# Kernel tuning notes

Measured on AMD Instinct MI355X. Metric: run time of the kernel, lower is better.

## Reference

```python
import jax, jax.numpy as jnp
import numpy as np

N = 50000      # nodes
E = 800000     # edges
D = 128        # input_dim
H = 128        # hidden_dim
OUT = 86       # output_dim (DDI classes)
P = 100000     # drug pairs
BN_EPS = 1e-5


def setup_inputs() -> dict:
    key = jax.random.key(0)
    ks = jax.random.split(key, 16)
    s = 0.05
    return {
        "x": jax.random.normal(ks[0], (N, D), jnp.float32),
        "edge_index": jax.random.randint(ks[1], (2, E), 0, N),
        "drug_pairs": jax.random.randint(ks[2], (P, 2), 0, N),
        # GCN layer 1 (input_dim -> hidden_dim) + BatchNorm params
        "W1": jax.random.normal(ks[3], (D, H), jnp.float32) * s,
        "b1": jnp.zeros((H,), jnp.float32),
        "gamma1": jnp.ones((H,), jnp.float32),
        "beta1": jnp.zeros((H,), jnp.float32),
        # GCN layer 2 (hidden -> hidden) + BatchNorm params
        "W2": jax.random.normal(ks[4], (H, H), jnp.float32) * s,
        "b2": jnp.zeros((H,), jnp.float32),
        "gamma2": jnp.ones((H,), jnp.float32),
        "beta2": jnp.zeros((H,), jnp.float32),
        # edge classifier MLP: Linear(2H,H) -> ReLU -> Linear(H,H//2) -> ReLU -> Linear(H//2,OUT)
        "Wc1": jax.random.normal(ks[5], (2 * H, H), jnp.float32) * s,
        "bc1": jnp.zeros((H,), jnp.float32),
        "Wc2": jax.random.normal(ks[6], (H, H // 2), jnp.float32) * s,
        "bc2": jnp.zeros((H // 2,), jnp.float32),
        "Wc3": jax.random.normal(ks[7], (H // 2, OUT), jnp.float32) * s,
        "bc3": jnp.zeros((OUT,), jnp.float32),
    }


def gcn_conv(h, W, b, src, dst, n):
    """PyG GCNConv: D^-1/2 (A + I) D^-1/2 (h @ W) + b, with self-loops added."""
    h = h @ W  # [N, H]
    ones = jnp.ones(src.shape[0], h.dtype)
    deg = jax.ops.segment_sum(ones, dst, num_segments=n) + 1.0  # in-degree + self loop
    dinv = jax.lax.rsqrt(deg)  # [N]
    coef = dinv[src] * dinv[dst]  # [E] edge normalization
    agg = jax.ops.segment_sum(h[src] * coef[:, None], dst, num_segments=n)
    agg = agg + h * (dinv * dinv)[:, None]  # self-loop contribution: deg_i^-1 * h_i
    return agg + b


def batch_norm(h, gamma, beta):
    # training-mode BatchNorm1d over node dim (biased variance)
    mean = jnp.mean(h, axis=0)
    var = jnp.mean((h - mean) ** 2, axis=0)
    return gamma * (h - mean) * jax.lax.rsqrt(var + BN_EPS) + beta


def reference(x, edge_index, drug_pairs, W1, b1, gamma1, beta1,
              W2, b2, gamma2, beta2, Wc1, bc1, Wc2, bc2, Wc3, bc3):
    src, dst = edge_index[0], edge_index[1]
    n = x.shape[0]
    # layer 1
    h = jax.nn.relu(batch_norm(gcn_conv(x, W1, b1, src, dst, n), gamma1, beta1))
    # layer 2
    h = jax.nn.relu(batch_norm(gcn_conv(h, W2, b2, src, dst, n), gamma2, beta2))
    # node-pair gather + concat -> edge classifier MLP (dropout = identity in eval)
    combined = jnp.concatenate([h[drug_pairs[:, 0]], h[drug_pairs[:, 1]]], axis=1)  # [P, 2H]
    z = jax.nn.relu(combined @ Wc1 + bc1)
    z = jax.nn.relu(z @ Wc2 + bc2)
    return z @ Wc3 + bc3  # [P, OUT]
```

## Files before the change

kernel.cpp:

```cpp
#include <hip/hip_runtime.h>
#include <cstdint>

#define N_NODES 50000
#define N_EDGES 800000
#define NPAIRS  100000

typedef unsigned short u16;
typedef unsigned int u32;
typedef _Float16 f16;
typedef short short8v __attribute__((ext_vector_type(8)));
typedef _Float16 h8 __attribute__((ext_vector_type(8)));
typedef _Float16 h4 __attribute__((ext_vector_type(4)));
typedef float f32x4 __attribute__((ext_vector_type(4)));

static __device__ __forceinline__ u16 f2bf(float f) {
  unsigned int u = __float_as_uint(f);
  u += 0x7FFF + ((u >> 16) & 1);
  return (u16)(u >> 16);
}


__global__ __launch_bounds__(256) void deg_count_k(const int* __restrict__ ei, int* __restrict__ deg, int E) {
  int e = blockIdx.x * 256 + threadIdx.x;
  if (e < E) atomicAdd(&deg[ei[E + e]], 1);
}

__global__ __launch_bounds__(256) void dinv_k(const int* __restrict__ deg, float* __restrict__ dinv, int n) {
  int i = blockIdx.x * 256 + threadIdx.x;
  if (i < n) dinv[i] = rsqrtf((float)deg[i] + 1.0f);
}

__global__ __launch_bounds__(1024) void scan_k(const int* __restrict__ deg, int* __restrict__ offs, int n) {
  __shared__ int wsum[16];
  __shared__ int wpre[16];
  __shared__ int run_s;
  int tid = threadIdx.x, lane = tid & 63, wid = tid >> 6;
  if (tid == 0) run_s = 0;
  __syncthreads();
  for (int base = 0; base < n; base += 4096) {
    int i4 = base + tid * 4;
    int4 v = make_int4(0, 0, 0, 0);
    if (i4 + 3 < n) v = *(const int4*)&deg[i4];
    else {
      if (i4 < n) v.x = deg[i4];
      if (i4 + 1 < n) v.y = deg[i4 + 1];
      if (i4 + 2 < n) v.z = deg[i4 + 2];
      if (i4 + 3 < n) v.w = deg[i4 + 3];
    }
    int tsum = v.x + v.y + v.z + v.w;
    int s = tsum;
#pragma unroll
    for (int d = 1; d < 64; d <<= 1) {
      int t = __shfl_up(s, d);
      if (lane >= d) s += t;
    }
    if (lane == 63) wsum[wid] = s;
    __syncthreads();
    if (tid == 0) {
      int acc = run_s;
#pragma unroll
      for (int w = 0; w < 16; w++) { wpre[w] = acc; acc += wsum[w]; }
      run_s = acc;
    }
    __syncthreads();
    int pre = wpre[wid] + (s - tsum);
    int4 o;
    o.x = pre; o.y = pre + v.x; o.z = o.y + v.y; o.w = o.z + v.z;
    if (i4 + 3 < n) *(int4*)&offs[i4] = o;
    else {
      if (i4 < n) offs[i4] = o.x;
      if (i4 + 1 < n) offs[i4 + 1] = o.y;
      if (i4 + 2 < n) offs[i4 + 2] = o.z;
      if (i4 + 3 < n) offs[i4 + 3] = o.w;
    }
    __syncthreads();
  }
  if (tid == 0) offs[n] = run_s;
}

__global__ __launch_bounds__(256) void fill_k(const int* __restrict__ ei, const int* __restrict__ offs,
                                              int* __restrict__ cursor, int* __restrict__ csr,
                                              float* __restrict__ csrc, const float* __restrict__ dinv, int E) {
  int e = blockIdx.x * 256 + threadIdx.x;
  if (e < E) {
    int s = ei[e], d = ei[E + e];
    int p = atomicAdd(&cursor[d], 1);
    int idx = offs[d] + p;
    csr[idx] = s;
    csrc[idx] = dinv[s];
  }
}

__global__ __launch_bounds__(256) void prep_w_k(const float* __restrict__ W1, const float* __restrict__ W2,
                                                const float* __restrict__ Wc1, const float* __restrict__ Wc2,
                                                const float* __restrict__ Wc3,
                                                f16* __restrict__ W1F, f16* __restrict__ W2F,
                                                u16* __restrict__ Wc1F, u16* __restrict__ Wc2F, u16* __restrict__ Wc3F) {
  int slot = blockIdx.x * 256 + threadIdx.x;
  int lane = slot & 63, j = lane & 15, kg = lane >> 4;
  if (slot < 2048) {
    int ks = (slot >> 6) & 3, nt = slot >> 8;
    int k0 = ks * 32 + kg * 8, c = nt * 16 + j;
#pragma unroll
    for (int e = 0; e < 8; e++) W1F[(size_t)slot * 8 + e] = (f16)W1[(k0 + e) * 128 + c];
  } else if (slot < 4096) {
    int s2 = slot - 2048;
    int ks = (s2 >> 6) & 3, nt = s2 >> 8;
    int k0 = ks * 32 + kg * 8, c = nt * 16 + j;
#pragma unroll
    for (int e = 0; e < 8; e++) W2F[(size_t)s2 * 8 + e] = (f16)W2[(k0 + e) * 128 + c];
  } else if (slot < 8192) {
    int s3 = slot - 4096;
    int ks = (s3 >> 6) & 7, nt = s3 >> 9;
    int k0 = ks * 32 + kg * 8, c = nt * 16 + j;
#pragma unroll
    for (int e = 0; e < 8; e++) Wc1F[(size_t)s3 * 8 + e] = f2bf(Wc1[(k0 + e) * 128 + c]);
  } else if (slot < 9216) {
    int s4 = slot - 8192;
    int ks = (s4 >> 6) & 3, nt = s4 >> 8;
    int k0 = ks * 32 + kg * 8, c = nt * 16 + j;
#pragma unroll
    for (int e = 0; e < 8; e++) Wc2F[(size_t)s4 * 8 + e] = f2bf(Wc2[(k0 + e) * 64 + c]);
  } else if (slot < 10240) {
    int s5 = slot - 9216;
    int ks = (s5 >> 6) & 1, nt = s5 >> 7;
    int k0 = ks * 32 + kg * 8, c = nt * 16 + j;
#pragma unroll
    for (int e = 0; e < 8; e++)
      Wc3F[(size_t)s5 * 8 + e] = f2bf((c < 86) ? Wc3[(k0 + e) * 86 + c] : 0.f);
  }
}


__global__ __launch_bounds__(256) void gemm_mfma_k(const float* __restrict__ A,
                                                   const float* __restrict__ scsh,
                                                   const f16* __restrict__ WF,
                                                   f16* __restrict__ outh, int n) {
  __shared__ f16 As[64 * 136];
  int tid = threadIdx.x;
  int row0 = blockIdx.x * 64;
#pragma unroll
  for (int it = 0; it < 8; it++) {
    int idx = it * 256 + tid;
    int r = idx >> 5, c4 = (idx & 31) * 4;
    int gr = row0 + r; if (gr >= n) gr = n - 1;
    float4 v = *(const float4*)&A[(size_t)gr * 128 + c4];
    if (scsh) {
      v.x = fmaxf(v.x * scsh[c4 + 0] + scsh[128 + c4 + 0], 0.f);
      v.y = fmaxf(v.y * scsh[c4 + 1] + scsh[128 + c4 + 1], 0.f);
      v.z = fmaxf(v.z * scsh[c4 + 2] + scsh[128 + c4 + 2], 0.f);
      v.w = fmaxf(v.w * scsh[c4 + 3] + scsh[128 + c4 + 3], 0.f);
    }
    h4 hv; hv[0] = (f16)v.x; hv[1] = (f16)v.y; hv[2] = (f16)v.z; hv[3] = (f16)v.w;
    *(h4*)&As[r * 136 + c4] = hv;
  }
  __syncthreads();
  int w = tid >> 6, lane = tid & 63, li = lane & 15, kg = lane >> 4;
  f32x4 acc[4][2];
#pragma unroll
  for (int mt = 0; mt < 4; mt++)
#pragma unroll
    for (int ntl = 0; ntl < 2; ntl++)
#pragma unroll
      for (int q = 0; q < 4; q++) acc[mt][ntl][q] = 0.f;
#pragma unroll
  for (int ks = 0; ks < 4; ks++) {
    h8 a[4];
#pragma unroll
    for (int mt = 0; mt < 4; mt++)
      a[mt] = *(const h8*)&As[(mt * 16 + li) * 136 + kg * 8 + ks * 32];
#pragma unroll
    for (int ntl = 0; ntl < 2; ntl++) {
      int nt = 2 * w + ntl;
      h8 b = *(const h8*)&WF[((size_t)(nt * 4 + ks) * 64 + lane) * 8];
#pragma unroll
      for (int mt = 0; mt < 4; mt++)
        acc[mt][ntl] = __builtin_amdgcn_mfma_f32_16x16x32_f16(a[mt], b, acc[mt][ntl], 0, 0, 0);
    }
  }
  __syncthreads();
#pragma unroll
  for (int mt = 0; mt < 4; mt++)
#pragma unroll
    for (int ntl = 0; ntl < 2; ntl++)
#pragma unroll
      for (int r = 0; r < 4; r++)
        As[(mt * 16 + kg * 4 + r) * 136 + (2 * w + ntl) * 16 + li] = (f16)acc[mt][ntl][r];
  __syncthreads();
#pragma unroll
  for (int it = 0; it < 4; it++) {
    int idx = it * 256 + tid;
    int r = idx >> 4, c8 = (idx & 15) * 8;
    int gr = row0 + r;
    if (gr < n) *(h8*)&outh[(size_t)gr * 128 + c8] = *(const h8*)&As[r * 136 + c8];
  }
}


__global__ __launch_bounds__(256) void agg_h_k(const f16* __restrict__ th, const float* __restrict__ dinv,
                                               const int* __restrict__ offs, const int* __restrict__ csr,
                                               const float* __restrict__ csrc,
                                               const float* __restrict__ bias, float* __restrict__ out, int n) {
  int node = blockIdx.x * 4 + (threadIdx.x >> 6);
  if (node >= n) return;
  int lane = threadIdx.x & 63;
  const u32* hu = (const u32*)th;
  float di = dinv[node];
  int e0 = offs[node], e1 = offs[node + 1];
  union CV { u32 u; f16 h[2]; };
  float a0x = 0.f, a0y = 0.f, a1x = 0.f, a1y = 0.f;
  float a2x = 0.f, a2y = 0.f, a3x = 0.f, a3y = 0.f;
  int e = e0;
  for (; e + 4 <= e1; e += 4) {
    int s0 = csr[e], s1 = csr[e + 1], s2 = csr[e + 2], s3 = csr[e + 3];
    float c0 = csrc[e], c1 = csrc[e + 1], c2 = csrc[e + 2], c3 = csrc[e + 3];
    CV v0, v1, v2, v3;
    v0.u = hu[(size_t)s0 * 64 + lane];
    v1.u = hu[(size_t)s1 * 64 + lane];
    v2.u = hu[(size_t)s2 * 64 + lane];
    v3.u = hu[(size_t)s3 * 64 + lane];
    a0x += c0 * (float)v0.h[0]; a0y += c0 * (float)v0.h[1];
    a1x += c1 * (float)v1.h[0]; a1y += c1 * (float)v1.h[1];
    a2x += c2 * (float)v2.h[0]; a2y += c2 * (float)v2.h[1];
    a3x += c3 * (float)v3.h[0]; a3y += c3 * (float)v3.h[1];
  }
  for (; e < e1; e++) {
    int s0 = csr[e];
    float c0 = csrc[e];
    CV v0; v0.u = hu[(size_t)s0 * 64 + lane];
    a0x += c0 * (float)v0.h[0]; a0y += c0 * (float)v0.h[1];
  }
  float sx = (a0x + a1x) + (a2x + a3x);
  float sy = (a0y + a1y) + (a2y + a3y);
  CV vs; vs.u = hu[(size_t)node * 64 + lane];
  float sc = di * di;
  float rx = di * sx + sc * (float)vs.h[0] + bias[lane * 2];
  float ry = di * sy + sc * (float)vs.h[1] + bias[lane * 2 + 1];
  float2 r; r.x = rx; r.y = ry;
  *(float2*)&out[(size_t)node * 128 + lane * 2] = r;
}


__global__ __launch_bounds__(256) void bn_stats_k(const float* __restrict__ h, float* __restrict__ sums, int n) {
  __shared__ float red[512];
  int tid = threadIdx.x;
  int c = tid & 127, half = tid >> 7;
  float s = 0.f, s2 = 0.f;
  for (int r = blockIdx.x * 2 + half; r < n; r += gridDim.x * 2) {
    float v = h[(size_t)r * 128 + c];
    s += v; s2 += v * v;
  }
  red[tid] = s; red[256 + tid] = s2;
  __syncthreads();
  if (half == 0) {
    s  = red[tid] + red[tid + 128];
    s2 = red[256 + tid] + red[256 + tid + 128];
    atomicAdd(&sums[c], s);
    atomicAdd(&sums[128 + c], s2);
  }
}

__global__ __launch_bounds__(128) void bn_fin_k(const float* __restrict__ sums, const float* __restrict__ gamma,
                                                const float* __restrict__ beta, float* __restrict__ scsh) {
  int c = threadIdx.x;
  const float inv_n = 1.0f / (float)N_NODES;
  float mean = sums[c] * inv_n;
  float var = sums[128 + c] * inv_n - mean * mean;
  float sc = gamma[c] * rsqrtf(var + 1e-5f);
  scsh[c] = sc;
  scsh[128 + c] = beta[c] - mean * sc;
}

__global__ __launch_bounds__(256) void bn_apply_bf16_k(const float* __restrict__ h, const float* __restrict__ scsh,
                                                       u16* __restrict__ hb) {
  int idx = blockIdx.x * 256 + threadIdx.x;
  int c0 = (idx & 31) * 4;
  float4 v = *(const float4*)&h[(size_t)idx * 4];
  ushort4 o;
  o.x = f2bf(fmaxf(v.x * scsh[c0 + 0] + scsh[128 + c0 + 0], 0.f));
  o.y = f2bf(fmaxf(v.y * scsh[c0 + 1] + scsh[128 + c0 + 1], 0.f));
  o.z = f2bf(fmaxf(v.z * scsh[c0 + 2] + scsh[128 + c0 + 2], 0.f));
  o.w = f2bf(fmaxf(v.w * scsh[c0 + 3] + scsh[128 + c0 + 3], 0.f));
  *(ushort4*)&hb[(size_t)idx * 4] = o;
}


#define SM_Z1 33792
#define SM_TOT (33792 + 17408)

__global__ __launch_bounds__(256) void classifier_k(const u16* __restrict__ hbf, const int* __restrict__ pairs,
    const u16* __restrict__ Wc1F, const float* __restrict__ bc1,
    const u16* __restrict__ Wc2F, const float* __restrict__ bc2,
    const u16* __restrict__ Wc3F, const float* __restrict__ bc3,
    float* __restrict__ out) {
  __shared__ __align__(16) char smem[SM_TOT];
  __shared__ int nodes[128];
  int tid = threadIdx.x;
  int p0 = blockIdx.x * 64;
  if (tid < 128) {
    int gi = p0 * 2 + tid;
    nodes[tid] = (gi < NPAIRS * 2) ? pairs[gi] : 0;
  }
  __syncthreads();
  int w = tid >> 6, lane = tid & 63;
  int li = lane & 15, kg = lane >> 4;

  {
    unsigned int* cmb = (unsigned int*)smem;
    for (int s = w * 32; s < w * 32 + 32; s++) {
      int nd = nodes[s];
      unsigned int v = ((const unsigned int*)hbf)[(size_t)nd * 64 + lane];
      cmb[(s >> 1) * 132 + (s & 1) * 64 + lane] = v;
    }
  }
  __syncthreads();

  {
    f32x4 acc[4][2];
#pragma unroll
    for (int ntl = 0; ntl < 2; ntl++) {
      float b = bc1[(2 * w + ntl) * 16 + li];
#pragma unroll
      for (int mt = 0; mt < 4; mt++)
#pragma unroll
        for (int q = 0; q < 4; q++) acc[mt][ntl][q] = b;
    }
    for (int ks = 0; ks < 8; ks++) {
      short8v a[4];
#pragma unroll
      for (int mt = 0; mt < 4; mt++)
        a[mt] = *(const short8v*)(smem + (mt * 16 + li) * 528 + kg * 16 + ks * 64);
#pragma unroll
      for (int ntl = 0; ntl < 2; ntl++) {
        int nt = 2 * w + ntl;
        short8v b = *(const short8v*)(Wc1F + ((size_t)(nt * 8 + ks) * 64 + lane) * 8);
#pragma unroll
        for (int mt = 0; mt < 4; mt++)
          acc[mt][ntl] = __builtin_amdgcn_mfma_f32_16x16x32_bf16(a[mt], b, acc[mt][ntl], 0, 0, 0);
      }
    }
#pragma unroll
    for (int mt = 0; mt < 4; mt++)
#pragma unroll
      for (int ntl = 0; ntl < 2; ntl++)
#pragma unroll
        for (int r = 0; r < 4; r++) {
          int row = mt * 16 + kg * 4 + r;
          int col = (2 * w + ntl) * 16 + li;
          *(u16*)(smem + SM_Z1 + row * 272 + col * 2) = f2bf(fmaxf(acc[mt][ntl][r], 0.f));
        }
  }
  __syncthreads();

  {
    f32x4 acc[4];
    float b = bc2[w * 16 + li];
#pragma unroll
    for (int mt = 0; mt < 4; mt++)
#pragma unroll
      for (int q = 0; q < 4; q++) acc[mt][q] = b;
    for (int ks = 0; ks < 4; ks++) {
      short8v a[4];
#pragma unroll
      for (int mt = 0; mt < 4; mt++)
        a[mt] = *(const short8v*)(smem + SM_Z1 + (mt * 16 + li) * 272 + kg * 16 + ks * 64);
      short8v bf = *(const short8v*)(Wc2F + ((size_t)(w * 4 + ks) * 64 + lane) * 8);
#pragma unroll
      for (int mt = 0; mt < 4; mt++)
        acc[mt] = __builtin_amdgcn_mfma_f32_16x16x32_bf16(a[mt], bf, acc[mt], 0, 0, 0);
    }
#pragma unroll
    for (int mt = 0; mt < 4; mt++)
#pragma unroll
      for (int r = 0; r < 4; r++) {
        int row = mt * 16 + kg * 4 + r;
        int col = w * 16 + li;
        *(u16*)(smem + row * 144 + col * 2) = f2bf(fmaxf(acc[mt][r], 0.f));
      }
  }
  __syncthreads();

  {
    f32x4 acc[4][2];
#pragma unroll
    for (int ntl = 0; ntl < 2; ntl++) {
      int col = (2 * w + ntl) * 16 + li;
      float b = (col < 86) ? bc3[col] : 0.f;
#pragma unroll
      for (int mt = 0; mt < 4; mt++)
#pragma unroll
        for (int q = 0; q < 4; q++) acc[mt][ntl][q] = b;
    }
    for (int ks = 0; ks < 2; ks++) {
      short8v a[4];
#pragma unroll
      for (int mt = 0; mt < 4; mt++)
        a[mt] = *(const short8v*)(smem + (mt * 16 + li) * 144 + kg * 16 + ks * 64);
#pragma unroll
      for (int ntl = 0; ntl < 2; ntl++) {
        int nt = 2 * w + ntl;
        short8v bf = *(const short8v*)(Wc3F + ((size_t)(nt * 2 + ks) * 64 + lane) * 8);
#pragma unroll
        for (int mt = 0; mt < 4; mt++)
          acc[mt][ntl] = __builtin_amdgcn_mfma_f32_16x16x32_bf16(a[mt], bf, acc[mt][ntl], 0, 0, 0);
      }
    }
#pragma unroll
    for (int mt = 0; mt < 4; mt++)
#pragma unroll
      for (int ntl = 0; ntl < 2; ntl++) {
        int col = (2 * w + ntl) * 16 + li;
        if (col < 86) {
#pragma unroll
          for (int r = 0; r < 4; r++) {
            int row = p0 + mt * 16 + kg * 4 + r;
            if (row < NPAIRS) out[(size_t)row * 86 + col] = acc[mt][ntl][r];
          }
        }
      }
  }
}


extern "C" void kernel_launch(void* const* d_in, const int* in_sizes, int n_in,
                              void* d_out, int out_size, void* d_ws, size_t ws_size,
                              hipStream_t stream) {
  (void)in_sizes; (void)n_in; (void)out_size; (void)ws_size;
  const float* x   = (const float*)d_in[0];
  const int*   ei  = (const int*)d_in[1];
  const int* pairs = (const int*)d_in[2];
  const float* W1  = (const float*)d_in[3];
  const float* b1  = (const float*)d_in[4];
  const float* g1  = (const float*)d_in[5];
  const float* be1 = (const float*)d_in[6];
  const float* W2  = (const float*)d_in[7];
  const float* b2  = (const float*)d_in[8];
  const float* g2  = (const float*)d_in[9];
  const float* be2 = (const float*)d_in[10];
  const float* Wc1 = (const float*)d_in[11];
  const float* bc1 = (const float*)d_in[12];
  const float* Wc2 = (const float*)d_in[13];
  const float* bc2 = (const float*)d_in[14];
  const float* Wc3 = (const float*)d_in[15];
  const float* bc3 = (const float*)d_in[16];
  float* out = (float*)d_out;

  size_t off = 0;
  auto alloc = [&](size_t bytes) -> char* {
    char* p = (char*)d_ws + off;
    off += (bytes + 255) & ~(size_t)255;
    return p;
  };
  int* deg      = (int*)alloc(N_NODES * 4);
  int* cursor   = (int*)alloc(N_NODES * 4);
  float* sums1  = (float*)alloc(256 * 4);
  float* sums2  = (float*)alloc(256 * 4);
  size_t zero_span = off;
  int* offs     = (int*)alloc((N_NODES + 1) * 4);
  int* csr      = (int*)alloc(N_EDGES * 4);
  float* csrc   = (float*)alloc(N_EDGES * 4);
  float* dinv   = (float*)alloc(N_NODES * 4);
  float* scsh1  = (float*)alloc(256 * 4);
  float* scsh2  = (float*)alloc(256 * 4);
  f16* W1F      = (f16*)alloc(2048 * 8 * 2);
  f16* W2F      = (f16*)alloc(2048 * 8 * 2);
  u16* Wc1F     = (u16*)alloc(4096 * 8 * 2);
  u16* Wc2F     = (u16*)alloc(1024 * 8 * 2);
  u16* Wc3F     = (u16*)alloc(1024 * 8 * 2);
  float* bufB   = (float*)alloc((size_t)N_NODES * 128 * 4);
  f16* th       = (f16*)alloc((size_t)N_NODES * 128 * 2);
  u16* hbf      = (u16*)th;

  hipMemsetAsync(d_ws, 0, zero_span, stream);
  deg_count_k<<<(N_EDGES + 255) / 256, 256, 0, stream>>>(ei, deg, N_EDGES);
  dinv_k<<<(N_NODES + 255) / 256, 256, 0, stream>>>(deg, dinv, N_NODES);
  scan_k<<<1, 1024, 0, stream>>>(deg, offs, N_NODES);
  fill_k<<<(N_EDGES + 255) / 256, 256, 0, stream>>>(ei, offs, cursor, csr, csrc, dinv, N_EDGES);
  prep_w_k<<<40, 256, 0, stream>>>(W1, W2, Wc1, Wc2, Wc3, W1F, W2F, Wc1F, Wc2F, Wc3F);

  gemm_mfma_k<<<(N_NODES + 63) / 64, 256, 0, stream>>>(x, nullptr, W1F, th, N_NODES);
  agg_h_k<<<N_NODES / 4, 256, 0, stream>>>(th, dinv, offs, csr, csrc, b1, bufB, N_NODES);
  bn_stats_k<<<256, 256, 0, stream>>>(bufB, sums1, N_NODES);
  bn_fin_k<<<1, 128, 0, stream>>>(sums1, g1, be1, scsh1);

  gemm_mfma_k<<<(N_NODES + 63) / 64, 256, 0, stream>>>(bufB, scsh1, W2F, th, N_NODES);
  agg_h_k<<<N_NODES / 4, 256, 0, stream>>>(th, dinv, offs, csr, csrc, b2, bufB, N_NODES);
  bn_stats_k<<<256, 256, 0, stream>>>(bufB, sums2, N_NODES);
  bn_fin_k<<<1, 128, 0, stream>>>(sums2, g2, be2, scsh2);
  bn_apply_bf16_k<<<N_NODES / 8, 256, 0, stream>>>(bufB, scsh2, hbf);

  classifier_k<<<(NPAIRS + 63) / 64, 256, 0, stream>>>(hbf, pairs, Wc1F, bc1, Wc2F, bc2, Wc3F, bc3, out);
}
```

Baseline: 397.4 us.

## Fuse preprocessing kernels, pack CSR entries, fuse BN stats into aggregation with fp16 storage

```diff
diff --git a/kernel.cpp b/kernel.cpp
--- a/kernel.cpp
+++ b/kernel.cpp
@@ -19,18 +19,62 @@
   return (u16)(u >> 16);
 }
 
-
-__global__ __launch_bounds__(256) void deg_count_k(const int* __restrict__ ei, int* __restrict__ deg, int E) {
-  int e = blockIdx.x * 256 + threadIdx.x;
-  if (e < E) atomicAdd(&deg[ei[E + e]], 1);
-}
-
-__global__ __launch_bounds__(256) void dinv_k(const int* __restrict__ deg, float* __restrict__ dinv, int n) {
-  int i = blockIdx.x * 256 + threadIdx.x;
-  if (i < n) dinv[i] = rsqrtf((float)deg[i] + 1.0f);
-}
-
-__global__ __launch_bounds__(1024) void scan_k(const int* __restrict__ deg, int* __restrict__ offs, int n) {
+static __device__ __forceinline__ float bits2f(u32 hi) {
+  union { u16 b; f16 h; } x;
+  x.b = (u16)hi;
+  return (float)x.h;
+}
+
+
+__global__ __launch_bounds__(256) void pre_k(const int* __restrict__ ei, int* __restrict__ deg, int* __restrict__ rank,
+                                             const float* __restrict__ W1, const float* __restrict__ W2,
+                                             const float* __restrict__ Wc1, const float* __restrict__ Wc2,
+                                             const float* __restrict__ Wc3,
+                                             f16* __restrict__ W1F, f16* __restrict__ W2F,
+                                             u16* __restrict__ Wc1F, u16* __restrict__ Wc2F, u16* __restrict__ Wc3F) {
+  int b = blockIdx.x;
+  if (b < N_EDGES / 256) {
+    int e = b * 256 + threadIdx.x;
+    rank[e] = atomicAdd(&deg[ei[N_EDGES + e]], 1);
+    return;
+  }
+  int slot = (b - N_EDGES / 256) * 256 + threadIdx.x;
+  int lane = slot & 63, j = lane & 15, kg = lane >> 4;
+  if (slot < 2048) {
+    int ks = (slot >> 6) & 3, nt = slot >> 8;
+    int k0 = ks * 32 + kg * 8, c = nt * 16 + j;
+#pragma unroll
+    for (int e = 0; e < 8; e++) W1F[(size_t)slot * 8 + e] = (f16)W1[(k0 + e) * 128 + c];
+  } else if (slot < 4096) {
+    int s2 = slot - 2048;
+    int ks = (s2 >> 6) & 3, nt = s2 >> 8;
+    int k0 = ks * 32 + kg * 8, c = nt * 16 + j;
+#pragma unroll
+    for (int e = 0; e < 8; e++) W2F[(size_t)s2 * 8 + e] = (f16)W2[(k0 + e) * 128 + c];
+  } else if (slot < 8192) {
+    int s3 = slot - 4096;
+    int ks = (s3 >> 6) & 7, nt = s3 >> 9;
+    int k0 = ks * 32 + kg * 8, c = nt * 16 + j;
+#pragma unroll
+    for (int e = 0; e < 8; e++) Wc1F[(size_t)s3 * 8 + e] = f2bf(Wc1[(k0 + e) * 128 + c]);
+  } else if (slot < 9216) {
+    int s4 = slot - 8192;
+    int ks = (s4 >> 6) & 3, nt = s4 >> 8;
+    int k0 = ks * 32 + kg * 8, c = nt * 16 + j;
+#pragma unroll
+    for (int e = 0; e < 8; e++) Wc2F[(size_t)s4 * 8 + e] = f2bf(Wc2[(k0 + e) * 64 + c]);
+  } else if (slot < 10240) {
+    int s5 = slot - 9216;
+    int ks = (s5 >> 6) & 1, nt = s5 >> 7;
+    int k0 = ks * 32 + kg * 8, c = nt * 16 + j;
+#pragma unroll
+    for (int e = 0; e < 8; e++)
+      Wc3F[(size_t)s5 * 8 + e] = f2bf((c < 86) ? Wc3[(k0 + e) * 86 + c] : 0.f);
+  }
+}
+
+__global__ __launch_bounds__(1024) void scan_k(const int* __restrict__ deg, int* __restrict__ offs,
+                                               float* __restrict__ dinv, int n) {
   __shared__ int wsum[16];
   __shared__ int wpre[16];
   __shared__ int run_s;
@@ -66,12 +110,19 @@
     int pre = wpre[wid] + (s - tsum);
     int4 o;
     o.x = pre; o.y = pre + v.x; o.z = o.y + v.y; o.w = o.z + v.z;
-    if (i4 + 3 < n) *(int4*)&offs[i4] = o;
-    else {
-      if (i4 < n) offs[i4] = o.x;
-      if (i4 + 1 < n) offs[i4 + 1] = o.y;
-      if (i4 + 2 < n) offs[i4 + 2] = o.z;
-      if (i4 + 3 < n) offs[i4 + 3] = o.w;
+    float4 dv;
+    dv.x = rsqrtf((float)v.x + 1.0f);
+    dv.y = rsqrtf((float)v.y + 1.0f);
+    dv.z = rsqrtf((float)v.z + 1.0f);
+    dv.w = rsqrtf((float)v.w + 1.0f);
+    if (i4 + 3 < n) {
+      *(int4*)&offs[i4] = o;
+      *(float4*)&dinv[i4] = dv;
+    } else {
+      if (i4 < n)     { offs[i4] = o.x;     dinv[i4] = dv.x; }
+      if (i4 + 1 < n) { offs[i4 + 1] = o.y; dinv[i4 + 1] = dv.y; }
+      if (i4 + 2 < n) { offs[i4 + 2] = o.z; dinv[i4 + 2] = dv.z; }
+      if (i4 + 3 < n) { offs[i4 + 3] = o.w; dinv[i4 + 3] = dv.w; }
     }
     __syncthreads();
   }
@@ -79,73 +130,52 @@
 }
 
 __global__ __launch_bounds__(256) void fill_k(const int* __restrict__ ei, const int* __restrict__ offs,
-                                              int* __restrict__ cursor, int* __restrict__ csr,
-                                              float* __restrict__ csrc, const float* __restrict__ dinv, int E) {
+                                              const int* __restrict__ rank, const float* __restrict__ dinv,
+                                              u32* __restrict__ csrp, int E) {
   int e = blockIdx.x * 256 + threadIdx.x;
   if (e < E) {
     int s = ei[e], d = ei[E + e];
-    int p = atomicAdd(&cursor[d], 1);
-    int idx = offs[d] + p;
-    csr[idx] = s;
-    csrc[idx] = dinv[s];
-  }
-}
-
-__global__ __launch_bounds__(256) void prep_w_k(const float* __restrict__ W1, const float* __restrict__ W2,
-                                                const float* __restrict__ Wc1, const float* __restrict__ Wc2,
-                                                const float* __restrict__ Wc3,
-                                                f16* __restrict__ W1F, f16* __restrict__ W2F,
-                                                u16* __restrict__ Wc1F, u16* __restrict__ Wc2F, u16* __restrict__ Wc3F) {
-  int slot = blockIdx.x * 256 + threadIdx.x;
-  int lane = slot & 63, j = lane & 15, kg = lane >> 4;
-  if (slot < 2048) {
-    int ks = (slot >> 6) & 3, nt = slot >> 8;
-    int k0 = ks * 32 + kg * 8, c = nt * 16 + j;
-#pragma unroll
-    for (int e = 0; e < 8; e++) W1F[(size_t)slot * 8 + e] = (f16)W1[(k0 + e) * 128 + c];
-  } else if (slot < 4096) {
-    int s2 = slot - 2048;
-    int ks = (s2 >> 6) & 3, nt = s2 >> 8;
-    int k0 = ks * 32 + kg * 8, c = nt * 16 + j;
-#pragma unroll
-    for (int e = 0; e < 8; e++) W2F[(size_t)s2 * 8 + e] = (f16)W2[(k0 + e) * 128 + c];
-  } else if (slot < 8192) {
-    int s3 = slot - 4096;
-    int ks = (s3 >> 6) & 7, nt = s3 >> 9;
-    int k0 = ks * 32 + kg * 8, c = nt * 16 + j;
-#pragma unroll
-    for (int e = 0; e < 8; e++) Wc1F[(size_t)s3 * 8 + e] = f2bf(Wc1[(k0 + e) * 128 + c]);
-  } else if (slot < 9216) {
-    int s4 = slot - 8192;
-    int ks = (s4 >> 6) & 3, nt = s4 >> 8;
-    int k0 = ks * 32 + kg * 8, c = nt * 16 + j;
-#pragma unroll
-    for (int e = 0; e < 8; e++) Wc2F[(size_t)s4 * 8 + e] = f2bf(Wc2[(k0 + e) * 64 + c]);
-  } else if (slot < 10240) {
-    int s5 = slot - 9216;
-    int ks = (s5 >> 6) & 1, nt = s5 >> 7;
-    int k0 = ks * 32 + kg * 8, c = nt * 16 + j;
-#pragma unroll
-    for (int e = 0; e < 8; e++)
-      Wc3F[(size_t)s5 * 8 + e] = f2bf((c < 86) ? Wc3[(k0 + e) * 86 + c] : 0.f);
-  }
-}
-
-
-__global__ __launch_bounds__(256) void gemm_mfma_k(const float* __restrict__ A,
-                                                   const float* __restrict__ scsh,
+    int idx = offs[d] + rank[e];
+    f16 hv = (f16)dinv[s];
+    u32 pack = (u32)(u16)s | ((u32)(*(u16*)&hv) << 16);
+    csrp[idx] = pack;
+  }
+}
+
+
+template<int MODE>
+__global__ __launch_bounds__(256) void gemm_mfma_k(const void* __restrict__ Ain,
+                                                   const float* __restrict__ sums,
+                                                   const float* __restrict__ gamma,
+                                                   const float* __restrict__ beta,
                                                    const f16* __restrict__ WF,
                                                    f16* __restrict__ outh, int n) {
   __shared__ f16 As[64 * 136];
+  __shared__ float scsh[256];
   int tid = threadIdx.x;
+  if (MODE == 1) {
+    if (tid < 128) {
+      const float inv_n = 1.0f / (float)N_NODES;
+      float mean = sums[tid] * inv_n;
+      float var = sums[128 + tid] * inv_n - mean * mean;
+      float sc = gamma[tid] * rsqrtf(var + 1e-5f);
+      scsh[tid] = sc;
+      scsh[128 + tid] = beta[tid] - mean * sc;
+    }
+    __syncthreads();
+  }
   int row0 = blockIdx.x * 64;
 #pragma unroll
   for (int it = 0; it < 8; it++) {
     int idx = it * 256 + tid;
     int r = idx >> 5, c4 = (idx & 31) * 4;
     int gr = row0 + r; if (gr >= n) gr = n - 1;
-    float4 v = *(const float4*)&A[(size_t)gr * 128 + c4];
-    if (scsh) {
+    float4 v;
+    if (MODE == 0) {
+      v = *(const float4*)&((const float*)Ain)[(size_t)gr * 128 + c4];
+    } else {
+      h4 hv4 = *(const h4*)&((const f16*)Ain)[(size_t)gr * 128 + c4];
+      v.x = (float)hv4[0]; v.y = (float)hv4[1]; v.z = (float)hv4[2]; v.w = (float)hv4[3];
       v.x = fmaxf(v.x * scsh[c4 + 0] + scsh[128 + c4 + 0], 0.f);
       v.y = fmaxf(v.y * scsh[c4 + 1] + scsh[128 + c4 + 1], 0.f);
       v.z = fmaxf(v.z * scsh[c4 + 2] + scsh[128 + c4 + 2], 0.f);
@@ -198,89 +228,89 @@
 
 
 __global__ __launch_bounds__(256) void agg_h_k(const f16* __restrict__ th, const float* __restrict__ dinv,
-                                               const int* __restrict__ offs, const int* __restrict__ csr,
-                                               const float* __restrict__ csrc,
-                                               const float* __restrict__ bias, float* __restrict__ out, int n) {
-  int node = blockIdx.x * 4 + (threadIdx.x >> 6);
-  if (node >= n) return;
-  int lane = threadIdx.x & 63;
+                                               const int* __restrict__ offs, const u32* __restrict__ csrp,
+                                               const float* __restrict__ bias, f16* __restrict__ outh,
+                                               float* __restrict__ sums, int n) {
+  int tid = threadIdx.x;
+  int lane = tid & 63, w = tid >> 6;
   const u32* hu = (const u32*)th;
-  float di = dinv[node];
-  int e0 = offs[node], e1 = offs[node + 1];
+  u32* ou = (u32*)outh;
+  float bx = bias[lane * 2], by = bias[lane * 2 + 1];
+  float s1x = 0.f, s1y = 0.f, q1x = 0.f, q1y = 0.f;
   union CV { u32 u; f16 h[2]; };
-  float a0x = 0.f, a0y = 0.f, a1x = 0.f, a1y = 0.f;
-  float a2x = 0.f, a2y = 0.f, a3x = 0.f, a3y = 0.f;
-  int e = e0;
-  for (; e + 4 <= e1; e += 4) {
-    int s0 = csr[e], s1 = csr[e + 1], s2 = csr[e + 2], s3 = csr[e + 3];
-    float c0 = csrc[e], c1 = csrc[e + 1], c2 = csrc[e + 2], c3 = csrc[e + 3];
-    CV v0, v1, v2, v3;
-    v0.u = hu[(size_t)s0 * 64 + lane];
-    v1.u = hu[(size_t)s1 * 64 + lane];
-    v2.u = hu[(size_t)s2 * 64 + lane];
-    v3.u = hu[(size_t)s3 * 64 + lane];
-    a0x += c0 * (float)v0.h[0]; a0y += c0 * (float)v0.h[1];
-    a1x += c1 * (float)v1.h[0]; a1y += c1 * (float)v1.h[1];
-    a2x += c2 * (float)v2.h[0]; a2y += c2 * (float)v2.h[1];
-    a3x += c3 * (float)v3.h[0]; a3y += c3 * (float)v3.h[1];
-  }
-  for (; e < e1; e++) {
-    int s0 = csr[e];
-    float c0 = csrc[e];
-    CV v0; v0.u = hu[(size_t)s0 * 64 + lane];
-    a0x += c0 * (float)v0.h[0]; a0y += c0 * (float)v0.h[1];
-  }
-  float sx = (a0x + a1x) + (a2x + a3x);
-  float sy = (a0y + a1y) + (a2y + a3y);
-  CV vs; vs.u = hu[(size_t)node * 64 + lane];
-  float sc = di * di;
-  float rx = di * sx + sc * (float)vs.h[0] + bias[lane * 2];
-  float ry = di * sy + sc * (float)vs.h[1] + bias[lane * 2 + 1];
-  float2 r; r.x = rx; r.y = ry;
-  *(float2*)&out[(size_t)node * 128 + lane * 2] = r;
-}
-
-
-__global__ __launch_bounds__(256) void bn_stats_k(const float* __restrict__ h, float* __restrict__ sums, int n) {
-  __shared__ float red[512];
+  for (int node = blockIdx.x * 4 + w; node < n; node += gridDim.x * 4) {
+    float di = dinv[node];
+    int e0 = offs[node], e1 = offs[node + 1];
+    float a0x = 0.f, a0y = 0.f, a1x = 0.f, a1y = 0.f;
+    float a2x = 0.f, a2y = 0.f, a3x = 0.f, a3y = 0.f;
+    int e = e0;
+    for (; e + 4 <= e1; e += 4) {
+      u32 p0 = csrp[e], p1 = csrp[e + 1], p2 = csrp[e + 2], p3 = csrp[e + 3];
+      float c0 = bits2f(p0 >> 16), c1 = bits2f(p1 >> 16);
+      float c2 = bits2f(p2 >> 16), c3 = bits2f(p3 >> 16);
+      CV v0, v1, v2, v3;
+      v0.u = hu[(size_t)(p0 & 0xFFFF) * 64 + lane];
+      v1.u = hu[(size_t)(p1 & 0xFFFF) * 64 + lane];
+      v2.u = hu[(size_t)(p2 & 0xFFFF) * 64 + lane];
+      v3.u = hu[(size_t)(p3 & 0xFFFF) * 64 + lane];
+      a0x += c0 * (float)v0.h[0]; a0y += c0 * (float)v0.h[1];
+      a1x += c1 * (float)v1.h[0]; a1y += c1 * (float)v1.h[1];
+      a2x += c2 * (float)v2.h[0]; a2y += c2 * (float)v2.h[1];
+      a3x += c3 * (float)v3.h[0]; a3y += c3 * (float)v3.h[1];
+    }
+    for (; e < e1; e++) {
+      u32 p0 = csrp[e];
+      float c0 = bits2f(p0 >> 16);
+      CV v0; v0.u = hu[(size_t)(p0 & 0xFFFF) * 64 + lane];
+      a0x += c0 * (float)v0.h[0]; a0y += c0 * (float)v0.h[1];
+    }
+    float sx = (a0x + a1x) + (a2x + a3x);
+    float sy = (a0y + a1y) + (a2y + a3y);
+    CV vs; vs.u = hu[(size_t)node * 64 + lane];
+    float sc = di * di;
+    float rx = di * sx + sc * (float)vs.h[0] + bx;
+    float ry = di * sy + sc * (float)vs.h[1] + by;
+    CV o; o.h[0] = (f16)rx; o.h[1] = (f16)ry;
+    ou[(size_t)node * 64 + lane] = o.u;
+    s1x += rx; q1x += rx * rx;
+    s1y += ry; q1y += ry * ry;
+  }
+  __shared__ float rsum[4][128];
+  __shared__ float rsq[4][128];
+  rsum[w][lane * 2] = s1x; rsum[w][lane * 2 + 1] = s1y;
+  rsq[w][lane * 2] = q1x;  rsq[w][lane * 2 + 1] = q1y;
+  __syncthreads();
+  if (tid < 128) {
+    float a = (rsum[0][tid] + rsum[1][tid]) + (rsum[2][tid] + rsum[3][tid]);
+    float b = (rsq[0][tid] + rsq[1][tid]) + (rsq[2][tid] + rsq[3][tid]);
+    atomicAdd(&sums[tid], a);
+    atomicAdd(&sums[128 + tid], b);
+  }
+}
+
+
+__global__ __launch_bounds__(256) void bn_apply_bf16_k(const f16* __restrict__ h, const float* __restrict__ sums,
+                                                       const float* __restrict__ gamma, const float* __restrict__ beta,
+                                                       u16* __restrict__ hb) {
+  __shared__ float scsh[256];
   int tid = threadIdx.x;
-  int c = tid & 127, half = tid >> 7;
-  float s = 0.f, s2 = 0.f;
-  for (int r = blockIdx.x * 2 + half; r < n; r += gridDim.x * 2) {
-    float v = h[(size_t)r * 128 + c];
-    s += v; s2 += v * v;
-  }
-  red[tid] = s; red[256 + tid] = s2;
-  __syncthreads();
-  if (half == 0) {
-    s  = red[tid] + red[tid + 128];
-    s2 = red[256 + tid] + red[256 + tid + 128];
-    atomicAdd(&sums[c], s);
-    atomicAdd(&sums[128 + c], s2);
-  }
-}
-
-__global__ __launch_bounds__(128) void bn_fin_k(const float* __restrict__ sums, const float* __restrict__ gamma,
-                                                const float* __restrict__ beta, float* __restrict__ scsh) {
-  int c = threadIdx.x;
-  const float inv_n = 1.0f / (float)N_NODES;
-  float mean = sums[c] * inv_n;
-  float var = sums[128 + c] * inv_n - mean * mean;
-  float sc = gamma[c] * rsqrtf(var + 1e-5f);
-  scsh[c] = sc;
-  scsh[128 + c] = beta[c] - mean * sc;
-}
-
-__global__ __launch_bounds__(256) void bn_apply_bf16_k(const float* __restrict__ h, const float* __restrict__ scsh,
-                                                       u16* __restrict__ hb) {
-  int idx = blockIdx.x * 256 + threadIdx.x;
+  if (tid < 128) {
+    const float inv_n = 1.0f / (float)N_NODES;
+    float mean = sums[tid] * inv_n;
+    float var = sums[128 + tid] * inv_n - mean * mean;
+    float sc = gamma[tid] * rsqrtf(var + 1e-5f);
+    scsh[tid] = sc;
+    scsh[128 + tid] = beta[tid] - mean * sc;
+  }
+  __syncthreads();
+  int idx = blockIdx.x * 256 + tid;
   int c0 = (idx & 31) * 4;
-  float4 v = *(const float4*)&h[(size_t)idx * 4];
+  h4 v4 = *(const h4*)&h[(size_t)idx * 4];
   ushort4 o;
-  o.x = f2bf(fmaxf(v.x * scsh[c0 + 0] + scsh[128 + c0 + 0], 0.f));
-  o.y = f2bf(fmaxf(v.y * scsh[c0 + 1] + scsh[128 + c0 + 1], 0.f));
-  o.z = f2bf(fmaxf(v.z * scsh[c0 + 2] + scsh[128 + c0 + 2], 0.f));
-  o.w = f2bf(fmaxf(v.w * scsh[c0 + 3] + scsh[128 + c0 + 3], 0.f));
+  o.x = f2bf(fmaxf((float)v4[0] * scsh[c0 + 0] + scsh[128 + c0 + 0], 0.f));
+  o.y = f2bf(fmaxf((float)v4[1] * scsh[c0 + 1] + scsh[128 + c0 + 1], 0.f));
+  o.z = f2bf(fmaxf((float)v4[2] * scsh[c0 + 2] + scsh[128 + c0 + 2], 0.f));
+  o.w = f2bf(fmaxf((float)v4[3] * scsh[c0 + 3] + scsh[128 + c0 + 3], 0.f));
   *(ushort4*)&hb[(size_t)idx * 4] = o;
 }
 
@@ -452,42 +482,35 @@
     return p;
   };
   int* deg      = (int*)alloc(N_NODES * 4);
-  int* cursor   = (int*)alloc(N_NODES * 4);
   float* sums1  = (float*)alloc(256 * 4);
   float* sums2  = (float*)alloc(256 * 4);
   size_t zero_span = off;
   int* offs     = (int*)alloc((N_NODES + 1) * 4);
-  int* csr      = (int*)alloc(N_EDGES * 4);
-  float* csrc   = (float*)alloc(N_EDGES * 4);
+  int* rank     = (int*)alloc(N_EDGES * 4);
+  u32* csrp     = (u32*)alloc(N_EDGES * 4);
   float* dinv   = (float*)alloc(N_NODES * 4);
-  float* scsh1  = (float*)alloc(256 * 4);
-  float* scsh2  = (float*)alloc(256 * 4);
   f16* W1F      = (f16*)alloc(2048 * 8 * 2);
   f16* W2F      = (f16*)alloc(2048 * 8 * 2);
   u16* Wc1F     = (u16*)alloc(4096 * 8 * 2);
   u16* Wc2F     = (u16*)alloc(1024 * 8 * 2);
   u16* Wc3F     = (u16*)alloc(1024 * 8 * 2);
-  float* bufB   = (float*)alloc((size_t)N_NODES * 128 * 4);
   f16* th       = (f16*)alloc((size_t)N_NODES * 128 * 2);
+  f16* hA       = (f16*)alloc((size_t)N_NODES * 128 * 2);
   u16* hbf      = (u16*)th;
 
   hipMemsetAsync(d_ws, 0, zero_span, stream);
-  deg_count_k<<<(N_EDGES + 255) / 256, 256, 0, stream>>>(ei, deg, N_EDGES);
-  dinv_k<<<(N_NODES + 255) / 256, 256, 0, stream>>>(deg, dinv, N_NODES);
-  scan_k<<<1, 1024, 0, stream>>>(deg, offs, N_NODES);
-  fill_k<<<(N_EDGES + 255) / 256, 256, 0, stream>>>(ei, offs, cursor, csr, csrc, dinv, N_EDGES);
-  prep_w_k<<<40, 256, 0, stream>>>(W1, W2, Wc1, Wc2, Wc3, W1F, W2F, Wc1F, Wc2F, Wc3F);
-
-  gemm_mfma_k<<<(N_NODES + 63) / 64, 256, 0, stream>>>(x, nullptr, W1F, th, N_NODES);
-  agg_h_k<<<N_NODES / 4, 256, 0, stream>>>(th, dinv, offs, csr, csrc, b1, bufB, N_NODES);
-  bn_stats_k<<<256, 256, 0, stream>>>(bufB, sums1, N_NODES);
-  bn_fin_k<<<1, 128, 0, stream>>>(sums1, g1, be1, scsh1);
-
-  gemm_mfma_k<<<(N_NODES + 63) / 64, 256, 0, stream>>>(bufB, scsh1, W2F, th, N_NODES);
-  agg_h_k<<<N_NODES / 4, 256, 0, stream>>>(th, dinv, offs, csr, csrc, b2, bufB, N_NODES);
-  bn_stats_k<<<256, 256, 0, stream>>>(bufB, sums2, N_NODES);
-  bn_fin_k<<<1, 128, 0, stream>>>(sums2, g2, be2, scsh2);
-  bn_apply_bf16_k<<<N_NODES / 8, 256, 0, stream>>>(bufB, scsh2, hbf);
+  pre_k<<<N_EDGES / 256 + 40, 256, 0, stream>>>(ei, deg, rank, W1, W2, Wc1, Wc2, Wc3,
+                                                W1F, W2F, Wc1F, Wc2F, Wc3F);
+  scan_k<<<1, 1024, 0, stream>>>(deg, offs, dinv, N_NODES);
+  fill_k<<<N_EDGES / 256, 256, 0, stream>>>(ei, offs, rank, dinv, csrp, N_EDGES);
+
+  gemm_mfma_k<0><<<(N_NODES + 63) / 64, 256, 0, stream>>>(x, nullptr, nullptr, nullptr, W1F, th, N_NODES);
+  agg_h_k<<<2048, 256, 0, stream>>>(th, dinv, offs, csrp, b1, hA, sums1, N_NODES);
+
+  gemm_mfma_k<1><<<(N_NODES + 63) / 64, 256, 0, stream>>>(hA, sums1, g1, be1, W2F, th, N_NODES);
+  agg_h_k<<<2048, 256, 0, stream>>>(th, dinv, offs, csrp, b2, hA, sums2, N_NODES);
+
+  bn_apply_bf16_k<<<(N_NODES * 128) / 1024, 256, 0, stream>>>(hA, sums2, g2, be2, hbf);
 
   classifier_k<<<(NPAIRS + 63) / 64, 256, 0, stream>>>(hbf, pairs, Wc1F, bc1, Wc2F, bc2, Wc3F, bc3, out);
 }
```

After: 390.2 us. No clear change (-1.8%).
